# Optimization experiments

Hardware: AMD Instinct MI355X
Metric: run time of the kernel (lower is better)

## Reference

```python
import jax, jax.numpy as jnp
import numpy as np

GROUP = 4  # SortAttn group
B, S, H, L = 64, 256, 1024, 4
GH = 2 * H // GROUP  # group_hidden


def _shuffle(a):
    # torch: x.transpose(-1,-2).contiguous().view(shape)
    return jnp.swapaxes(a, -1, -2).reshape(a.shape)


def _sort_attn(h, w0, w1, w2, w3):
    # h: (B,H). torch.sort(x, dim=1, stable=True) over hidden dim.
    b, hs = h.shape
    se = jnp.stack((h, jnp.sort(h, axis=1)), axis=1)          # (B,2,H)
    a = jnp.einsum('bth,oh->bto', se, w0)                     # Linear(H,H,no bias)
    a = a.reshape(b, GROUP, GH)                                # Flatten+Unflatten
    a = _shuffle(a)
    a = jnp.einsum('bgh,oh->bgo', a, w1)                      # Linear(GH,GH)
    a = _shuffle(a)
    a = jax.nn.relu(jnp.einsum('bgh,oh->bgo', a, w2))         # Linear(GH,GH)+ReLU
    a = a.reshape(b, 2 * hs) @ w3.T                           # Linear(2H,H)
    return h * jax.nn.sigmoid(a)


def _gru_cell(x, h, wih, whh, bih, bhh):
    gi = x @ wih.T + bih                                       # (B,3H)
    gh = h @ whh.T + bhh
    ir, iz, inn = jnp.split(gi, 3, axis=-1)
    hr, hz, hn = jnp.split(gh, 3, axis=-1)
    r = jax.nn.sigmoid(ir + hr)
    z = jax.nn.sigmoid(iz + hz)
    n = jnp.tanh(inn + r * hn)
    return (1.0 - z) * n + z * h


def setup_inputs() -> dict:
    key = jax.random.key(0)
    ks = jax.random.split(key, 10)
    sc = 1.0 / np.sqrt(H)
    return {
        'x': jax.random.normal(ks[0], (B, S, H), jnp.float32),
        'hidden0': jnp.zeros((L, 1, H), jnp.float32),
        'W_ih': jax.random.normal(ks[1], (L, 3 * H, H), jnp.float32) * sc,
        'W_hh': jax.random.normal(ks[2], (L, 3 * H, H), jnp.float32) * sc,
        'b_ih': jax.random.normal(ks[3], (L, 3 * H), jnp.float32) * sc,
        'b_hh': jax.random.normal(ks[4], (L, 3 * H), jnp.float32) * sc,
        'aw0': jax.random.normal(ks[5], (L, H, H), jnp.float32) * sc,
        'aw1': jax.random.normal(ks[6], (L, GH, GH), jnp.float32) * (1.0 / np.sqrt(GH)),
        'aw2': jax.random.normal(ks[7], (L, GH, GH), jnp.float32) * (1.0 / np.sqrt(GH)),
        'aw3': jax.random.normal(ks[8], (L, H, 2 * H), jnp.float32) * (1.0 / np.sqrt(2 * H)),
    }


def reference(x, hidden0, W_ih, W_hh, b_ih, b_hh, aw0, aw1, aw2, aw3):
    b = x.shape[0]
    nl = W_ih.shape[0]
    # hidden_0 * ones(1,B,1) -> broadcast to (L,B,H)
    h0 = jnp.broadcast_to(hidden0, (nl, b, hidden0.shape[-1]))

    def step(h, xt):
        inp = xt
        new = []
        for l in range(nl):
            hl = _gru_cell(inp, h[l], W_ih[l], W_hh[l], b_ih[l], b_hh[l])
            hl = _sort_attn(hl, aw0[l], aw1[l], aw2[l], aw3[l])
            new.append(hl)
            inp = hl
        return jnp.stack(new, 0), inp

    hT, outs = jax.lax.scan(step, h0, jnp.swapaxes(x, 0, 1))  # outs: (S,B,H)
    return jnp.swapaxes(outs, 0, 1), hT
```

## Files before the change

kernel.cpp:

```cpp
#include <hip/hip_runtime.h>
#include <hip/hip_bf16.h>

typedef __bf16 bf16_t;
typedef bf16_t bf16x8 __attribute__((ext_vector_type(8)));
typedef float  f32x4  __attribute__((ext_vector_type(4)));

#define NB 64
#define NS 256
#define NH 1024
#define NL 4
#define G3H 3072

__device__ __forceinline__ f32x4 mfma16(bf16x8 a, bf16x8 b, f32x4 c) {
    return __builtin_amdgcn_mfma_f32_16x16x32_bf16(a, b, c, 0, 0, 0);
}

__device__ __forceinline__ float sigmoidf_(float x) {
    return 1.0f / (1.0f + expf(-x));
}

struct P {
    const float* x;
    const float* b_ih;
    const float* b_hh;
    float* out;
    const bf16_t* Wih;
    const bf16_t* Whh;
    const bf16_t* w0;
    const bf16_t* w1;
    const bf16_t* w2;
    const bf16_t* w3;
    float*  h_fp;
    bf16_t* h_bf;
    float*  hprime;
    bf16_t* se;
    bf16_t* sA0;
    bf16_t* sA1;
    bf16_t* a2;
    bf16_t* outbuf;
};

struct ConvArgs {
    const float* src[6];
    bf16_t* dst[6];
    long n[6];
    const float* hidden0;
    float* h_fp;
    bf16_t* h_bf;
};

__global__ void __launch_bounds__(256) convert_kernel(ConvArgs a) {
    const long tid = (long)blockIdx.x * 256 + threadIdx.x;
    const long stride = (long)gridDim.x * 256;
    for (int i = 0; i < 6; ++i) {
        const float* s = a.src[i];
        bf16_t* d = a.dst[i];
        const long n = a.n[i];
        for (long j = tid * 4; j < n; j += stride * 4) {
            float4 v = *(const float4*)(s + j);
            d[j + 0] = (bf16_t)v.x;
            d[j + 1] = (bf16_t)v.y;
            d[j + 2] = (bf16_t)v.z;
            d[j + 3] = (bf16_t)v.w;
        }
    }
    for (long j = tid; j < (long)NL * NB * NH; j += stride) {
        int l = (int)(j >> 16);
        int c = (int)(j & (NH - 1));
        float v = a.hidden0[l * NH + c];
        a.h_fp[j] = v;
        a.h_bf[j] = (bf16_t)v;
    }
}

__global__ void __launch_bounds__(256) k_gru(P p, int s) {
    const int l = blockIdx.x >> 6;
    const int t = s - l;
    if (t < 0 || t >= NS) return;
    const int wj = blockIdx.x & 63;
    const int tid = threadIdx.x;
    const int wave = tid >> 6, lane = tid & 63;
    const int lane15 = lane & 15, quad = lane >> 4, kq = quad * 8;

    const bf16_t* Wih_l = p.Wih + (size_t)l * G3H * NH;
    const bf16_t* Whh_l = p.Whh + (size_t)l * G3H * NH;
    const float* bih_l = p.b_ih + l * G3H;
    const float* bhh_l = p.b_hh + l * G3H;
    const float*  hfp_l = p.h_fp + (size_t)l * NB * NH;
    const bf16_t* hbf_l = p.h_bf + (size_t)l * NB * NH;
    float*  hpr_l = p.hprime + (size_t)l * NB * NH;
    bf16_t* se_l  = p.se + (size_t)l * 2 * NB * NH;

    const int c0 = wj * 16;
    const int m0 = wave * 16;
    const int arow = m0 + lane15;
    const bf16_t* inp_l = (l > 0)
        ? (p.outbuf + ((size_t)(t & 1) * NL + (l - 1)) * NB * NH) : nullptr;
    const float* xrow = p.x + ((size_t)arow * NS + t) * NH;

    f32x4 acc[6] = {};
    for (int k0 = 0; k0 < NH; k0 += 32) {
        const int k = k0 + kq;
        bf16x8 a_i;
        if (l == 0) {
            float4 f0 = *(const float4*)(xrow + k);
            float4 f1 = *(const float4*)(xrow + k + 4);
            a_i[0] = (bf16_t)f0.x; a_i[1] = (bf16_t)f0.y;
            a_i[2] = (bf16_t)f0.z; a_i[3] = (bf16_t)f0.w;
            a_i[4] = (bf16_t)f1.x; a_i[5] = (bf16_t)f1.y;
            a_i[6] = (bf16_t)f1.z; a_i[7] = (bf16_t)f1.w;
        } else {
            a_i = *(const bf16x8*)(inp_l + (size_t)arow * NH + k);
        }
        bf16x8 a_h = *(const bf16x8*)(hbf_l + (size_t)arow * NH + k);
#pragma unroll
        for (int g = 0; g < 3; ++g) {
            bf16x8 bi = *(const bf16x8*)(Wih_l + (size_t)(g * NH + c0 + lane15) * NH + k);
            bf16x8 bh = *(const bf16x8*)(Whh_l + (size_t)(g * NH + c0 + lane15) * NH + k);
            acc[g]     = mfma16(a_i, bi, acc[g]);
            acc[3 + g] = mfma16(a_h, bh, acc[3 + g]);
        }
    }
    const int c = c0 + lane15;
#pragma unroll
    for (int i = 0; i < 4; ++i) {
        const int m = m0 + quad * 4 + i;
        float ir  = acc[0][i] + bih_l[c];
        float iz  = acc[1][i] + bih_l[NH + c];
        float inn = acc[2][i] + bih_l[2 * NH + c];
        float hr  = acc[3][i] + bhh_l[c];
        float hz  = acc[4][i] + bhh_l[NH + c];
        float hn  = acc[5][i] + bhh_l[2 * NH + c];
        float r = sigmoidf_(ir + hr);
        float z = sigmoidf_(iz + hz);
        float n = tanhf(inn + r * hn);
        float hprev = hfp_l[(size_t)m * NH + c];
        float hp = (1.0f - z) * n + z * hprev;
        hpr_l[(size_t)m * NH + c] = hp;
        se_l[(size_t)(m * 2) * NH + c] = (bf16_t)hp;
    }
}

__global__ void __launch_bounds__(256) k_sort(P p, int s) {
    const int l = blockIdx.x >> 6;
    const int t = s - l;
    if (t < 0 || t >= NS) return;
    const int b = blockIdx.x & 63;
    const int tid = threadIdx.x;
    const float* hpr_l = p.hprime + (size_t)l * NB * NH;
    bf16_t* se_l = p.se + (size_t)l * 2 * NB * NH;

    __shared__ float sbuf[NH];
    const float* src = hpr_l + (size_t)b * NH;
    for (int i = tid; i < NH; i += 256) sbuf[i] = src[i];
    __syncthreads();
    for (int kk = 2; kk <= NH; kk <<= 1) {
        for (int j = kk >> 1; j > 0; j >>= 1) {
#pragma unroll
            for (int bb = 0; bb < 4; ++bb) {
                const int i = bb * 256 + tid;
                const int ixj = i ^ j;
                if (ixj > i) {
                    float va = sbuf[i], vb = sbuf[ixj];
                    bool up = ((i & kk) == 0);
                    if (up ? (va > vb) : (va < vb)) {
                        sbuf[i] = vb; sbuf[ixj] = va;
                    }
                }
            }
            __syncthreads();
        }
    }
    bf16_t* dst = se_l + (size_t)(b * 2 + 1) * NH;
    for (int i = tid; i < NH; i += 256) dst[i] = (bf16_t)sbuf[i];
}

__global__ void __launch_bounds__(256) k_a0(P p, int s) {
    const int l = blockIdx.x >> 6;
    const int t = s - l;
    if (t < 0 || t >= NS) return;
    const int wj = blockIdx.x & 63;
    const int tid = threadIdx.x;
    const int wave = tid >> 6, lane = tid & 63;
    const int lane15 = lane & 15, quad = lane >> 4, kq = quad * 8;
    const bf16_t* w0_l = p.w0 + (size_t)l * NH * NH;
    const bf16_t* se_l = p.se + (size_t)l * 2 * NB * NH;
    bf16_t* sA0_l = p.sA0 + (size_t)l * NB * 2048;

    const int mhalf = wj >> 5;
    const int c0 = (wj & 31) * 32;
    const int r0 = mhalf * 64 + wave * 16;
    f32x4 acc0 = {}, acc1 = {};
    for (int k0 = 0; k0 < NH; k0 += 32) {
        const int k = k0 + kq;
        bf16x8 a  = *(const bf16x8*)(se_l + (size_t)(r0 + lane15) * NH + k);
        bf16x8 b0 = *(const bf16x8*)(w0_l + (size_t)(c0 + lane15) * NH + k);
        bf16x8 b1 = *(const bf16x8*)(w0_l + (size_t)(c0 + 16 + lane15) * NH + k);
        acc0 = mfma16(a, b0, acc0);
        acc1 = mfma16(a, b1, acc1);
    }
#pragma unroll
    for (int i = 0; i < 4; ++i) {
        const int r = r0 + quad * 4 + i;
        const int bidx = r >> 1, tt = r & 1;
        const int o0 = c0 + lane15;
        const int j0 = tt * NH + o0;
        sA0_l[(size_t)bidx * 2048 + ((j0 & 511) * 4 + (j0 >> 9))] = (bf16_t)acc0[i];
        const int j1 = tt * NH + o0 + 16;
        sA0_l[(size_t)bidx * 2048 + ((j1 & 511) * 4 + (j1 >> 9))] = (bf16_t)acc1[i];
    }
}

__global__ void __launch_bounds__(256) k_a1(P p, int s) {
    const int l = blockIdx.x >> 6;
    const int t = s - l;
    if (t < 0 || t >= NS) return;
    const int wj = blockIdx.x & 63;
    const int tid = threadIdx.x;
    const int wave = tid >> 6, lane = tid & 63;
    const int lane15 = lane & 15, quad = lane >> 4, kq = quad * 8;
    const bf16_t* w1_l = p.w1 + (size_t)l * 512 * 512;
    const bf16_t* sA0_l = p.sA0 + (size_t)l * NB * 2048;
    bf16_t* sA1_l = p.sA1 + (size_t)l * NB * 2048;

    const int mblk = wj >> 4;
    const int c0 = (wj & 15) * 32;
    const int r0 = mblk * 64 + wave * 16;
    f32x4 acc0 = {}, acc1 = {};
    for (int k0 = 0; k0 < 512; k0 += 32) {
        const int k = k0 + kq;
        bf16x8 a  = *(const bf16x8*)(sA0_l + (size_t)(r0 + lane15) * 512 + k);
        bf16x8 b0 = *(const bf16x8*)(w1_l + (size_t)(c0 + lane15) * 512 + k);
        bf16x8 b1 = *(const bf16x8*)(w1_l + (size_t)(c0 + 16 + lane15) * 512 + k);
        acc0 = mfma16(a, b0, acc0);
        acc1 = mfma16(a, b1, acc1);
    }
#pragma unroll
    for (int i = 0; i < 4; ++i) {
        const int rr = r0 + quad * 4 + i;
        const int bidx = rr >> 2, g = rr & 3;
        const int o0 = c0 + lane15;
        sA1_l[(size_t)bidx * 2048 + o0 * 4 + g]        = (bf16_t)acc0[i];
        sA1_l[(size_t)bidx * 2048 + (o0 + 16) * 4 + g] = (bf16_t)acc1[i];
    }
}

__global__ void __launch_bounds__(256) k_a2(P p, int s) {
    const int l = blockIdx.x >> 6;
    const int t = s - l;
    if (t < 0 || t >= NS) return;
    const int wj = blockIdx.x & 63;
    const int tid = threadIdx.x;
    const int wave = tid >> 6, lane = tid & 63;
    const int lane15 = lane & 15, quad = lane >> 4, kq = quad * 8;
    const bf16_t* w2_l = p.w2 + (size_t)l * 512 * 512;
    const bf16_t* sA1_l = p.sA1 + (size_t)l * NB * 2048;
    bf16_t* a2_l = p.a2 + (size_t)l * NB * 2048;

    const int mblk = wj >> 4;
    const int c0 = (wj & 15) * 32;
    const int r0 = mblk * 64 + wave * 16;
    f32x4 acc0 = {}, acc1 = {};
    for (int k0 = 0; k0 < 512; k0 += 32) {
        const int k = k0 + kq;
        bf16x8 a  = *(const bf16x8*)(sA1_l + (size_t)(r0 + lane15) * 512 + k);
        bf16x8 b0 = *(const bf16x8*)(w2_l + (size_t)(c0 + lane15) * 512 + k);
        bf16x8 b1 = *(const bf16x8*)(w2_l + (size_t)(c0 + 16 + lane15) * 512 + k);
        acc0 = mfma16(a, b0, acc0);
        acc1 = mfma16(a, b1, acc1);
    }
#pragma unroll
    for (int i = 0; i < 4; ++i) {
        const int rr = r0 + quad * 4 + i;
        const int o0 = c0 + lane15;
        float v0 = acc0[i] > 0.0f ? acc0[i] : 0.0f;
        float v1 = acc1[i] > 0.0f ? acc1[i] : 0.0f;
        a2_l[(size_t)rr * 512 + o0]      = (bf16_t)v0;
        a2_l[(size_t)rr * 512 + o0 + 16] = (bf16_t)v1;
    }
}

__global__ void __launch_bounds__(256) k_a3(P p, int s) {
    const int l = blockIdx.x >> 6;
    const int t = s - l;
    if (t < 0 || t >= NS) return;
    const int wj = blockIdx.x & 63;
    const int tid = threadIdx.x;
    const int wave = tid >> 6, lane = tid & 63;
    const int lane15 = lane & 15, quad = lane >> 4, kq = quad * 8;
    const bf16_t* w3_l = p.w3 + (size_t)l * NH * 2048;
    const bf16_t* a2_l = p.a2 + (size_t)l * NB * 2048;
    const float* hpr_l = p.hprime + (size_t)l * NB * NH;
    float*  hfp_l = p.h_fp + (size_t)l * NB * NH;
    bf16_t* hbf_l = p.h_bf + (size_t)l * NB * NH;

    const int c0 = wj * 16;
    const int m0 = wave * 16;
    f32x4 acc = {};
    for (int k0 = 0; k0 < 2048; k0 += 32) {
        const int k = k0 + kq;
        bf16x8 a = *(const bf16x8*)(a2_l + (size_t)(m0 + lane15) * 2048 + k);
        bf16x8 b = *(const bf16x8*)(w3_l + (size_t)(c0 + lane15) * 2048 + k);
        acc = mfma16(a, b, acc);
    }
    const int c = c0 + lane15;
    bf16_t* ob = (l < NL - 1)
        ? (p.outbuf + ((size_t)(t & 1) * NL + l) * NB * NH) : nullptr;
#pragma unroll
    for (int i = 0; i < 4; ++i) {
        const int m = m0 + quad * 4 + i;
        float sg = sigmoidf_(acc[i]);
        float val = hpr_l[(size_t)m * NH + c] * sg;
        hfp_l[(size_t)m * NH + c] = val;
        hbf_l[(size_t)m * NH + c] = (bf16_t)val;
        if (l < NL - 1) {
            ob[(size_t)m * NH + c] = (bf16_t)val;
        } else {
            p.out[((size_t)m * NS + t) * NH + c] = val;
        }
        if (t == NS - 1) {
            p.out[(size_t)NB * NS * NH + ((size_t)l * NB + m) * NH + c] = val;
        }
    }
}

extern "C" void kernel_launch(void* const* d_in, const int* in_sizes, int n_in,
                              void* d_out, int out_size, void* d_ws, size_t ws_size,
                              hipStream_t stream) {
    const float* x       = (const float*)d_in[0];
    const float* hidden0 = (const float*)d_in[1];
    const float* Wih_f   = (const float*)d_in[2];
    const float* Whh_f   = (const float*)d_in[3];
    const float* bih     = (const float*)d_in[4];
    const float* bhh     = (const float*)d_in[5];
    const float* aw0     = (const float*)d_in[6];
    const float* aw1     = (const float*)d_in[7];
    const float* aw2     = (const float*)d_in[8];
    const float* aw3     = (const float*)d_in[9];

    char* ws = (char*)d_ws;
    size_t off = 0;
    auto alloc = [&](size_t bytes) -> void* {
        void* r = ws + off;
        off = (off + bytes + 255) & ~(size_t)255;
        return r;
    };

    const long nWih = (long)NL * G3H * NH;
    const long nWhh = (long)NL * G3H * NH;
    const long nw0  = (long)NL * NH * NH;
    const long nw1  = (long)NL * 512 * 512;
    const long nw2  = (long)NL * 512 * 512;
    const long nw3  = (long)NL * NH * 2048;

    P p;
    p.x = x; p.b_ih = bih; p.b_hh = bhh; p.out = (float*)d_out;
    p.Wih = (bf16_t*)alloc((size_t)nWih * 2);
    p.Whh = (bf16_t*)alloc((size_t)nWhh * 2);
    p.w0  = (bf16_t*)alloc((size_t)nw0 * 2);
    p.w1  = (bf16_t*)alloc((size_t)nw1 * 2);
    p.w2  = (bf16_t*)alloc((size_t)nw2 * 2);
    p.w3  = (bf16_t*)alloc((size_t)nw3 * 2);
    p.h_fp   = (float*) alloc((size_t)NL * NB * NH * 4);
    p.h_bf   = (bf16_t*)alloc((size_t)NL * NB * NH * 2);
    p.hprime = (float*) alloc((size_t)NL * NB * NH * 4);
    p.se     = (bf16_t*)alloc((size_t)NL * 2 * NB * NH * 2);
    p.sA0    = (bf16_t*)alloc((size_t)NL * NB * 2048 * 2);
    p.sA1    = (bf16_t*)alloc((size_t)NL * NB * 2048 * 2);
    p.a2     = (bf16_t*)alloc((size_t)NL * NB * 2048 * 2);
    p.outbuf = (bf16_t*)alloc((size_t)2 * NL * NB * NH * 2);

    ConvArgs ca;
    ca.src[0] = Wih_f; ca.dst[0] = (bf16_t*)p.Wih; ca.n[0] = nWih;
    ca.src[1] = Whh_f; ca.dst[1] = (bf16_t*)p.Whh; ca.n[1] = nWhh;
    ca.src[2] = aw0;   ca.dst[2] = (bf16_t*)p.w0;  ca.n[2] = nw0;
    ca.src[3] = aw1;   ca.dst[3] = (bf16_t*)p.w1;  ca.n[3] = nw1;
    ca.src[4] = aw2;   ca.dst[4] = (bf16_t*)p.w2;  ca.n[4] = nw2;
    ca.src[5] = aw3;   ca.dst[5] = (bf16_t*)p.w3;  ca.n[5] = nw3;
    ca.hidden0 = hidden0;
    ca.h_fp = p.h_fp;
    ca.h_bf = p.h_bf;

    convert_kernel<<<dim3(2048), dim3(256), 0, stream>>>(ca);

    for (int s = 0; s < NS + NL - 1; ++s) {
        k_gru <<<dim3(NL * 64), dim3(256), 0, stream>>>(p, s);
        k_sort<<<dim3(NL * 64), dim3(256), 0, stream>>>(p, s);
        k_a0  <<<dim3(NL * 64), dim3(256), 0, stream>>>(p, s);
        k_a1  <<<dim3(NL * 64), dim3(256), 0, stream>>>(p, s);
        k_a2  <<<dim3(NL * 64), dim3(256), 0, stream>>>(p, s);
        k_a3  <<<dim3(NL * 64), dim3(256), 0, stream>>>(p, s);
    }
}
```

Measured before the change: 31.07 ms.

## Fuse per-step stage kernels into one persistent cooperative kernel with grid syncs

Replaces the six kernel launches per wavefront step (about 1550 launches in total) with a single cooperative kernel that loops over steps and separates stages with grid.sync. Blocks grow to 512 threads: the GRU stage splits input and hidden GEMMs across the two halves of the block, and the final projection splits K in two, with partial sums combined through shared memory. The a0/a1/a2 stages are retiled to one 16-column MFMA tile per wave. This removes launch gaps between the tiny dependent stages, but adds grid-wide barrier cost and requires all 256 blocks to be co-resident.

```diff
diff --git a/kernel.cpp b/kernel.cpp
--- a/kernel.cpp
+++ b/kernel.cpp
@@ -1,5 +1,8 @@
 #include <hip/hip_runtime.h>
 #include <hip/hip_bf16.h>
+#include <hip/hip_cooperative_groups.h>
+
+namespace cg = cooperative_groups;
 
 typedef __bf16 bf16_t;
 typedef bf16_t bf16x8 __attribute__((ext_vector_type(8)));
@@ -73,113 +76,130 @@
     }
 }
 
-__global__ void __launch_bounds__(256) k_gru(P p, int s) {
+__device__ __forceinline__ void st_gru(const P& p, int s, float* smem) {
     const int l = blockIdx.x >> 6;
     const int t = s - l;
     if (t < 0 || t >= NS) return;
     const int wj = blockIdx.x & 63;
     const int tid = threadIdx.x;
     const int wave = tid >> 6, lane = tid & 63;
+    const int half = wave >> 2, ws = wave & 3;
     const int lane15 = lane & 15, quad = lane >> 4, kq = quad * 8;
 
-    const bf16_t* Wih_l = p.Wih + (size_t)l * G3H * NH;
-    const bf16_t* Whh_l = p.Whh + (size_t)l * G3H * NH;
-    const float* bih_l = p.b_ih + l * G3H;
-    const float* bhh_l = p.b_hh + l * G3H;
-    const float*  hfp_l = p.h_fp + (size_t)l * NB * NH;
-    const bf16_t* hbf_l = p.h_bf + (size_t)l * NB * NH;
-    float*  hpr_l = p.hprime + (size_t)l * NB * NH;
-    bf16_t* se_l  = p.se + (size_t)l * 2 * NB * NH;
-
     const int c0 = wj * 16;
-    const int m0 = wave * 16;
+    const int m0 = ws * 16;
     const int arow = m0 + lane15;
-    const bf16_t* inp_l = (l > 0)
-        ? (p.outbuf + ((size_t)(t & 1) * NL + (l - 1)) * NB * NH) : nullptr;
-    const float* xrow = p.x + ((size_t)arow * NS + t) * NH;
-
-    f32x4 acc[6] = {};
-    for (int k0 = 0; k0 < NH; k0 += 32) {
-        const int k = k0 + kq;
-        bf16x8 a_i;
-        if (l == 0) {
+
+    const bf16_t* W = (half ? p.Whh : p.Wih) + (size_t)l * G3H * NH;
+    const bf16_t* brow0 = W + (size_t)(0 * NH + c0 + lane15) * NH;
+    const bf16_t* brow1 = W + (size_t)(1 * NH + c0 + lane15) * NH;
+    const bf16_t* brow2 = W + (size_t)(2 * NH + c0 + lane15) * NH;
+
+    f32x4 acc0 = {}, acc1 = {}, acc2 = {};
+
+    if (half == 0 && l == 0) {
+        const float* xrow = p.x + ((size_t)arow * NS + t) * NH;
+        for (int k0 = 0; k0 < NH; k0 += 32) {
+            const int k = k0 + kq;
             float4 f0 = *(const float4*)(xrow + k);
             float4 f1 = *(const float4*)(xrow + k + 4);
-            a_i[0] = (bf16_t)f0.x; a_i[1] = (bf16_t)f0.y;
-            a_i[2] = (bf16_t)f0.z; a_i[3] = (bf16_t)f0.w;
-            a_i[4] = (bf16_t)f1.x; a_i[5] = (bf16_t)f1.y;
-            a_i[6] = (bf16_t)f1.z; a_i[7] = (bf16_t)f1.w;
-        } else {
-            a_i = *(const bf16x8*)(inp_l + (size_t)arow * NH + k);
-        }
-        bf16x8 a_h = *(const bf16x8*)(hbf_l + (size_t)arow * NH + k);
-#pragma unroll
-        for (int g = 0; g < 3; ++g) {
-            bf16x8 bi = *(const bf16x8*)(Wih_l + (size_t)(g * NH + c0 + lane15) * NH + k);
-            bf16x8 bh = *(const bf16x8*)(Whh_l + (size_t)(g * NH + c0 + lane15) * NH + k);
-            acc[g]     = mfma16(a_i, bi, acc[g]);
-            acc[3 + g] = mfma16(a_h, bh, acc[3 + g]);
-        }
-    }
-    const int c = c0 + lane15;
-#pragma unroll
-    for (int i = 0; i < 4; ++i) {
-        const int m = m0 + quad * 4 + i;
-        float ir  = acc[0][i] + bih_l[c];
-        float iz  = acc[1][i] + bih_l[NH + c];
-        float inn = acc[2][i] + bih_l[2 * NH + c];
-        float hr  = acc[3][i] + bhh_l[c];
-        float hz  = acc[4][i] + bhh_l[NH + c];
-        float hn  = acc[5][i] + bhh_l[2 * NH + c];
-        float r = sigmoidf_(ir + hr);
-        float z = sigmoidf_(iz + hz);
-        float n = tanhf(inn + r * hn);
-        float hprev = hfp_l[(size_t)m * NH + c];
-        float hp = (1.0f - z) * n + z * hprev;
-        hpr_l[(size_t)m * NH + c] = hp;
-        se_l[(size_t)(m * 2) * NH + c] = (bf16_t)hp;
-    }
-}
-
-__global__ void __launch_bounds__(256) k_sort(P p, int s) {
+            bf16x8 a;
+            a[0] = (bf16_t)f0.x; a[1] = (bf16_t)f0.y;
+            a[2] = (bf16_t)f0.z; a[3] = (bf16_t)f0.w;
+            a[4] = (bf16_t)f1.x; a[5] = (bf16_t)f1.y;
+            a[6] = (bf16_t)f1.z; a[7] = (bf16_t)f1.w;
+            acc0 = mfma16(a, *(const bf16x8*)(brow0 + k), acc0);
+            acc1 = mfma16(a, *(const bf16x8*)(brow1 + k), acc1);
+            acc2 = mfma16(a, *(const bf16x8*)(brow2 + k), acc2);
+        }
+    } else {
+        const bf16_t* ap = half
+            ? (p.h_bf + (size_t)l * NB * NH + (size_t)arow * NH)
+            : (p.outbuf + ((size_t)(t & 1) * NL + (l - 1)) * NB * NH + (size_t)arow * NH);
+        for (int k0 = 0; k0 < NH; k0 += 32) {
+            const int k = k0 + kq;
+            bf16x8 a = *(const bf16x8*)(ap + k);
+            acc0 = mfma16(a, *(const bf16x8*)(brow0 + k), acc0);
+            acc1 = mfma16(a, *(const bf16x8*)(brow1 + k), acc1);
+            acc2 = mfma16(a, *(const bf16x8*)(brow2 + k), acc2);
+        }
+    }
+
+    if (half == 1) {
+        float* sl = smem + ws * 768 + lane * 4;
+#pragma unroll
+        for (int i = 0; i < 4; ++i) {
+            sl[i]       = acc0[i];
+            sl[256 + i] = acc1[i];
+            sl[512 + i] = acc2[i];
+        }
+    }
+    __syncthreads();
+    if (half == 0) {
+        const float* bih_l = p.b_ih + l * G3H;
+        const float* bhh_l = p.b_hh + l * G3H;
+        const float* hfp_l = p.h_fp + (size_t)l * NB * NH;
+        float*  hpr_l = p.hprime + (size_t)l * NB * NH;
+        bf16_t* se_l  = p.se + (size_t)l * 2 * NB * NH;
+        const int c = c0 + lane15;
+        const float* sl = smem + ws * 768 + lane * 4;
+        const float b0 = bih_l[c], b1 = bih_l[NH + c], b2 = bih_l[2 * NH + c];
+        const float d0 = bhh_l[c], d1 = bhh_l[NH + c], d2 = bhh_l[2 * NH + c];
+#pragma unroll
+        for (int i = 0; i < 4; ++i) {
+            const int m = m0 + quad * 4 + i;
+            float ir  = acc0[i] + b0;
+            float iz  = acc1[i] + b1;
+            float inn = acc2[i] + b2;
+            float hr  = sl[i]       + d0;
+            float hz  = sl[256 + i] + d1;
+            float hn  = sl[512 + i] + d2;
+            float r = sigmoidf_(ir + hr);
+            float z = sigmoidf_(iz + hz);
+            float n = tanhf(inn + r * hn);
+            float hprev = hfp_l[(size_t)m * NH + c];
+            float hp = (1.0f - z) * n + z * hprev;
+            hpr_l[(size_t)m * NH + c] = hp;
+            se_l[(size_t)(m * 2) * NH + c] = (bf16_t)hp;
+        }
+    }
+}
+
+__device__ __forceinline__ void st_sort(const P& p, int s, float* smem) {
     const int l = blockIdx.x >> 6;
     const int t = s - l;
     if (t < 0 || t >= NS) return;
     const int b = blockIdx.x & 63;
     const int tid = threadIdx.x;
-    const float* hpr_l = p.hprime + (size_t)l * NB * NH;
-    bf16_t* se_l = p.se + (size_t)l * 2 * NB * NH;
-
-    __shared__ float sbuf[NH];
-    const float* src = hpr_l + (size_t)b * NH;
-    for (int i = tid; i < NH; i += 256) sbuf[i] = src[i];
+    const float* src = p.hprime + (size_t)l * NB * NH + (size_t)b * NH;
+    for (int i = tid; i < NH; i += 512) smem[i] = src[i];
     __syncthreads();
     for (int kk = 2; kk <= NH; kk <<= 1) {
         for (int j = kk >> 1; j > 0; j >>= 1) {
 #pragma unroll
-            for (int bb = 0; bb < 4; ++bb) {
-                const int i = bb * 256 + tid;
+            for (int bb = 0; bb < 2; ++bb) {
+                const int i = bb * 512 + tid;
                 const int ixj = i ^ j;
                 if (ixj > i) {
-                    float va = sbuf[i], vb = sbuf[ixj];
+                    float va = smem[i], vb = smem[ixj];
                     bool up = ((i & kk) == 0);
                     if (up ? (va > vb) : (va < vb)) {
-                        sbuf[i] = vb; sbuf[ixj] = va;
+                        smem[i] = vb; smem[ixj] = va;
                     }
                 }
             }
             __syncthreads();
         }
     }
-    bf16_t* dst = se_l + (size_t)(b * 2 + 1) * NH;
-    for (int i = tid; i < NH; i += 256) dst[i] = (bf16_t)sbuf[i];
-}
-
-__global__ void __launch_bounds__(256) k_a0(P p, int s) {
-    const int l = blockIdx.x >> 6;
-    const int t = s - l;
-    if (t < 0 || t >= NS) return;
-    const int wj = blockIdx.x & 63;
+    bf16_t* dst = p.se + (size_t)l * 2 * NB * NH + (size_t)(b * 2 + 1) * NH;
+    for (int i = tid; i < NH; i += 512) dst[i] = (bf16_t)smem[i];
+}
+
+__device__ __forceinline__ void st_a0(const P& p, int s) {
+    const int l = blockIdx.x >> 6;
+    const int t = s - l;
+    if (t < 0 || t >= NS) return;
+    const int cj = blockIdx.x & 63;
     const int tid = threadIdx.x;
     const int wave = tid >> 6, lane = tid & 63;
     const int lane15 = lane & 15, quad = lane >> 4, kq = quad * 8;
@@ -187,31 +207,25 @@
     const bf16_t* se_l = p.se + (size_t)l * 2 * NB * NH;
     bf16_t* sA0_l = p.sA0 + (size_t)l * NB * 2048;
 
-    const int mhalf = wj >> 5;
-    const int c0 = (wj & 31) * 32;
-    const int r0 = mhalf * 64 + wave * 16;
-    f32x4 acc0 = {}, acc1 = {};
+    const int c0 = cj * 16;
+    const int r0 = wave * 16;
+    const bf16_t* arow = se_l + (size_t)(r0 + lane15) * NH;
+    const bf16_t* brow = w0_l + (size_t)(c0 + lane15) * NH;
+    f32x4 acc = {};
     for (int k0 = 0; k0 < NH; k0 += 32) {
         const int k = k0 + kq;
-        bf16x8 a  = *(const bf16x8*)(se_l + (size_t)(r0 + lane15) * NH + k);
-        bf16x8 b0 = *(const bf16x8*)(w0_l + (size_t)(c0 + lane15) * NH + k);
-        bf16x8 b1 = *(const bf16x8*)(w0_l + (size_t)(c0 + 16 + lane15) * NH + k);
-        acc0 = mfma16(a, b0, acc0);
-        acc1 = mfma16(a, b1, acc1);
+        acc = mfma16(*(const bf16x8*)(arow + k), *(const bf16x8*)(brow + k), acc);
     }
 #pragma unroll
     for (int i = 0; i < 4; ++i) {
         const int r = r0 + quad * 4 + i;
         const int bidx = r >> 1, tt = r & 1;
-        const int o0 = c0 + lane15;
-        const int j0 = tt * NH + o0;
-        sA0_l[(size_t)bidx * 2048 + ((j0 & 511) * 4 + (j0 >> 9))] = (bf16_t)acc0[i];
-        const int j1 = tt * NH + o0 + 16;
-        sA0_l[(size_t)bidx * 2048 + ((j1 & 511) * 4 + (j1 >> 9))] = (bf16_t)acc1[i];
-    }
-}
-
-__global__ void __launch_bounds__(256) k_a1(P p, int s) {
+        const int j0 = tt * NH + c0 + lane15;
+        sA0_l[(size_t)bidx * 2048 + ((j0 & 511) * 4 + (j0 >> 9))] = (bf16_t)acc[i];
+    }
+}
+
+__device__ __forceinline__ void st_a1(const P& p, int s) {
     const int l = blockIdx.x >> 6;
     const int t = s - l;
     if (t < 0 || t >= NS) return;
@@ -223,29 +237,26 @@
     const bf16_t* sA0_l = p.sA0 + (size_t)l * NB * 2048;
     bf16_t* sA1_l = p.sA1 + (size_t)l * NB * 2048;
 
-    const int mblk = wj >> 4;
-    const int c0 = (wj & 15) * 32;
-    const int r0 = mblk * 64 + wave * 16;
-    f32x4 acc0 = {}, acc1 = {};
+    const int mhalf = wj >> 5;
+    const int c0 = (wj & 31) * 16;
+    const int r0 = mhalf * 128 + wave * 16;
+    const bf16_t* arow = sA0_l + (size_t)(r0 + lane15) * 512;
+    const bf16_t* brow = w1_l + (size_t)(c0 + lane15) * 512;
+    f32x4 acc = {};
     for (int k0 = 0; k0 < 512; k0 += 32) {
         const int k = k0 + kq;
-        bf16x8 a  = *(const bf16x8*)(sA0_l + (size_t)(r0 + lane15) * 512 + k);
-        bf16x8 b0 = *(const bf16x8*)(w1_l + (size_t)(c0 + lane15) * 512 + k);
-        bf16x8 b1 = *(const bf16x8*)(w1_l + (size_t)(c0 + 16 + lane15) * 512 + k);
-        acc0 = mfma16(a, b0, acc0);
-        acc1 = mfma16(a, b1, acc1);
+        acc = mfma16(*(const bf16x8*)(arow + k), *(const bf16x8*)(brow + k), acc);
     }
 #pragma unroll
     for (int i = 0; i < 4; ++i) {
         const int rr = r0 + quad * 4 + i;
         const int bidx = rr >> 2, g = rr & 3;
         const int o0 = c0 + lane15;
-        sA1_l[(size_t)bidx * 2048 + o0 * 4 + g]        = (bf16_t)acc0[i];
-        sA1_l[(size_t)bidx * 2048 + (o0 + 16) * 4 + g] = (bf16_t)acc1[i];
-    }
-}
-
-__global__ void __launch_bounds__(256) k_a2(P p, int s) {
+        sA1_l[(size_t)bidx * 2048 + o0 * 4 + g] = (bf16_t)acc[i];
+    }
+}
+
+__device__ __forceinline__ void st_a2(const P& p, int s) {
     const int l = blockIdx.x >> 6;
     const int t = s - l;
     if (t < 0 || t >= NS) return;
@@ -257,70 +268,91 @@
     const bf16_t* sA1_l = p.sA1 + (size_t)l * NB * 2048;
     bf16_t* a2_l = p.a2 + (size_t)l * NB * 2048;
 
-    const int mblk = wj >> 4;
-    const int c0 = (wj & 15) * 32;
-    const int r0 = mblk * 64 + wave * 16;
-    f32x4 acc0 = {}, acc1 = {};
+    const int mhalf = wj >> 5;
+    const int c0 = (wj & 31) * 16;
+    const int r0 = mhalf * 128 + wave * 16;
+    const bf16_t* arow = sA1_l + (size_t)(r0 + lane15) * 512;
+    const bf16_t* brow = w2_l + (size_t)(c0 + lane15) * 512;
+    f32x4 acc = {};
     for (int k0 = 0; k0 < 512; k0 += 32) {
         const int k = k0 + kq;
-        bf16x8 a  = *(const bf16x8*)(sA1_l + (size_t)(r0 + lane15) * 512 + k);
-        bf16x8 b0 = *(const bf16x8*)(w2_l + (size_t)(c0 + lane15) * 512 + k);
-        bf16x8 b1 = *(const bf16x8*)(w2_l + (size_t)(c0 + 16 + lane15) * 512 + k);
-        acc0 = mfma16(a, b0, acc0);
-        acc1 = mfma16(a, b1, acc1);
+        acc = mfma16(*(const bf16x8*)(arow + k), *(const bf16x8*)(brow + k), acc);
     }
 #pragma unroll
     for (int i = 0; i < 4; ++i) {
         const int rr = r0 + quad * 4 + i;
         const int o0 = c0 + lane15;
-        float v0 = acc0[i] > 0.0f ? acc0[i] : 0.0f;
-        float v1 = acc1[i] > 0.0f ? acc1[i] : 0.0f;
-        a2_l[(size_t)rr * 512 + o0]      = (bf16_t)v0;
-        a2_l[(size_t)rr * 512 + o0 + 16] = (bf16_t)v1;
-    }
-}
-
-__global__ void __launch_bounds__(256) k_a3(P p, int s) {
+        float v = acc[i] > 0.0f ? acc[i] : 0.0f;
+        a2_l[(size_t)rr * 512 + o0] = (bf16_t)v;
+    }
+}
+
+__device__ __forceinline__ void st_a3(const P& p, int s, float* smem) {
     const int l = blockIdx.x >> 6;
     const int t = s - l;
     if (t < 0 || t >= NS) return;
     const int wj = blockIdx.x & 63;
     const int tid = threadIdx.x;
     const int wave = tid >> 6, lane = tid & 63;
+    const int kg = wave >> 2, ws = wave & 3;
     const int lane15 = lane & 15, quad = lane >> 4, kq = quad * 8;
     const bf16_t* w3_l = p.w3 + (size_t)l * NH * 2048;
     const bf16_t* a2_l = p.a2 + (size_t)l * NB * 2048;
-    const float* hpr_l = p.hprime + (size_t)l * NB * NH;
-    float*  hfp_l = p.h_fp + (size_t)l * NB * NH;
-    bf16_t* hbf_l = p.h_bf + (size_t)l * NB * NH;
 
     const int c0 = wj * 16;
-    const int m0 = wave * 16;
+    const int m0 = ws * 16;
+    const int kb = kg * 1024;
+    const bf16_t* arow = a2_l + (size_t)(m0 + lane15) * 2048 + kb;
+    const bf16_t* brow = w3_l + (size_t)(c0 + lane15) * 2048 + kb;
     f32x4 acc = {};
-    for (int k0 = 0; k0 < 2048; k0 += 32) {
+    for (int k0 = 0; k0 < 1024; k0 += 32) {
         const int k = k0 + kq;
-        bf16x8 a = *(const bf16x8*)(a2_l + (size_t)(m0 + lane15) * 2048 + k);
-        bf16x8 b = *(const bf16x8*)(w3_l + (size_t)(c0 + lane15) * 2048 + k);
-        acc = mfma16(a, b, acc);
-    }
-    const int c = c0 + lane15;
-    bf16_t* ob = (l < NL - 1)
-        ? (p.outbuf + ((size_t)(t & 1) * NL + l) * NB * NH) : nullptr;
-#pragma unroll
-    for (int i = 0; i < 4; ++i) {
-        const int m = m0 + quad * 4 + i;
-        float sg = sigmoidf_(acc[i]);
-        float val = hpr_l[(size_t)m * NH + c] * sg;
-        hfp_l[(size_t)m * NH + c] = val;
-        hbf_l[(size_t)m * NH + c] = (bf16_t)val;
-        if (l < NL - 1) {
-            ob[(size_t)m * NH + c] = (bf16_t)val;
-        } else {
-            p.out[((size_t)m * NS + t) * NH + c] = val;
-        }
-        if (t == NS - 1) {
-            p.out[(size_t)NB * NS * NH + ((size_t)l * NB + m) * NH + c] = val;
-        }
+        acc = mfma16(*(const bf16x8*)(arow + k), *(const bf16x8*)(brow + k), acc);
+    }
+    if (kg == 1) {
+        float* sl = smem + (ws * 64 + lane) * 4;
+#pragma unroll
+        for (int i = 0; i < 4; ++i) sl[i] = acc[i];
+    }
+    __syncthreads();
+    if (kg == 0) {
+        const float* hpr_l = p.hprime + (size_t)l * NB * NH;
+        float*  hfp_l = p.h_fp + (size_t)l * NB * NH;
+        bf16_t* hbf_l = p.h_bf + (size_t)l * NB * NH;
+        const float* sl = smem + (ws * 64 + lane) * 4;
+        const int c = c0 + lane15;
+        bf16_t* ob = (l < NL - 1)
+            ? (p.outbuf + ((size_t)(t & 1) * NL + l) * NB * NH) : nullptr;
+#pragma unroll
+        for (int i = 0; i < 4; ++i) {
+            const int m = m0 + quad * 4 + i;
+            float v = acc[i] + sl[i];
+            float sg = sigmoidf_(v);
+            float val = hpr_l[(size_t)m * NH + c] * sg;
+            hfp_l[(size_t)m * NH + c] = val;
+            hbf_l[(size_t)m * NH + c] = (bf16_t)val;
+            if (l < NL - 1) {
+                ob[(size_t)m * NH + c] = (bf16_t)val;
+            } else {
+                p.out[((size_t)m * NS + t) * NH + c] = val;
+            }
+            if (t == NS - 1) {
+                p.out[(size_t)NB * NS * NH + ((size_t)l * NB + m) * NH + c] = val;
+            }
+        }
+    }
+}
+
+__global__ void __launch_bounds__(512) fused_kernel(P p) {
+    __shared__ float smem[3072];
+    cg::grid_group grid = cg::this_grid();
+    for (int s = 0; s < NS + NL - 1; ++s) {
+        st_gru(p, s, smem);   grid.sync();
+        st_sort(p, s, smem);  grid.sync();
+        st_a0(p, s);          grid.sync();
+        st_a1(p, s);          grid.sync();
+        st_a2(p, s);          grid.sync();
+        st_a3(p, s, smem);    grid.sync();
     }
 }
 
@@ -383,12 +415,7 @@
 
     convert_kernel<<<dim3(2048), dim3(256), 0, stream>>>(ca);
 
-    for (int s = 0; s < NS + NL - 1; ++s) {
-        k_gru <<<dim3(NL * 64), dim3(256), 0, stream>>>(p, s);
-        k_sort<<<dim3(NL * 64), dim3(256), 0, stream>>>(p, s);
-        k_a0  <<<dim3(NL * 64), dim3(256), 0, stream>>>(p, s);
-        k_a1  <<<dim3(NL * 64), dim3(256), 0, stream>>>(p, s);
-        k_a2  <<<dim3(NL * 64), dim3(256), 0, stream>>>(p, s);
-        k_a3  <<<dim3(NL * 64), dim3(256), 0, stream>>>(p, s);
-    }
-}
+    void* kargs[] = { (void*)&p };
+    hipLaunchCooperativeKernel((const void*)fused_kernel, dim3(256), dim3(512),
+                               kargs, 0, stream);
+}
```

New measurement: 72.14 ms. 132% more time.
